# Kernel optimization log

Hardware: AMD Instinct MI355X
Metric: run time of the kernel (lower is better)

Reference implementation:

```python
import jax, jax.numpy as jnp
import numpy as np

NQ = 10          # qubits per register
DIM = 2 ** NQ    # 1024 amplitudes
N_CLS = 10       # canonical images (one per class)
N = 16384        # batch of samples
IMG = 28 * 28    # 784 pixels, zero-padded to DIM


def setup_inputs() -> dict:
    key = jax.random.key(0)
    k1, k2, k3 = jax.random.split(key, 3)
    z_re = jax.random.normal(k1, (N, DIM), dtype=jnp.float32)
    z_im = jax.random.normal(k2, (N, DIM), dtype=jnp.float32)
    # inputs are quantum states -> L2-normalize the complex vectors
    nrm = jnp.sqrt(jnp.sum(z_re * z_re + z_im * z_im, axis=1, keepdims=True))
    z_re = z_re / nrm
    z_im = z_im / nrm
    canon = jax.random.uniform(k3, (N_CLS, 1, 28, 28), dtype=jnp.float32)
    return {"z_re": z_re, "z_im": z_im, "canon": canon}


def reference(z_re, z_im, canon):
    # reshape_norm_padding: flatten, zero-pad to 2^nq, L2-normalize (real amplitudes)
    ref = canon.reshape(N_CLS, IMG)
    ref = jnp.pad(ref, ((0, 0), (0, DIM - IMG)))                  # [C, DIM]
    ref = ref / jnp.linalg.norm(ref, axis=1, keepdims=True)
    # Swap test: <Z_anc> = |<val|ref>|^2. ref is real, so with val = z_re + i*z_im:
    #   <val|ref> = (z_re @ ref^T) - i*(z_im @ ref^T)
    s_re = jnp.einsum('nd,cd->nc', z_re, ref)                     # [N, C]
    s_im = jnp.einsum('nd,cd->nc', z_im, ref)                     # [N, C]
    return s_re * s_re + s_im * s_im                              # [N, C] float32
```

## Files before the change

### kernel.cpp

```cpp
#include <hip/hip_runtime.h>

#define DIM     1024
#define N_CLS   10
#define NROWS   16384
#define IMG     784

#define NF4      196
#define NF4_PAD  224
#define NSTEP    7
#define LSTRIDE  224

#define WAVES_PER_BLK 8
#define ROWS_PER_BLK  16

typedef float f32x4 __attribute__((ext_vector_type(4)));
typedef float f32x2 __attribute__((ext_vector_type(2)));

static __device__ __forceinline__ f32x2 lo2(f32x4 v) {
  return __builtin_shufflevector(v, v, 0, 1);
}
static __device__ __forceinline__ f32x2 hi2(f32x4 v) {
  return __builtin_shufflevector(v, v, 2, 3);
}

static __device__ __forceinline__ void pk_fma(f32x2& acc, f32x2 a, f32x2 b) {
  asm("v_pk_fma_f32 %0, %1, %2, %0" : "+v"(acc) : "v"(a), "v"(b));
}

#define DPP_ADD(ctrl, rmask, bmask)                                           \
  x += __int_as_float(__builtin_amdgcn_update_dpp(                            \
      0, __float_as_int(x), ctrl, rmask, bmask, true));

__device__ __forceinline__ float wave64_sum(float x) {
  DPP_ADD(0x111, 0xf, 0xf)
  DPP_ADD(0x112, 0xf, 0xf)
  DPP_ADD(0x114, 0xf, 0xe)
  DPP_ADD(0x118, 0xf, 0xc)
  DPP_ADD(0x142, 0xa, 0xf)
  DPP_ADD(0x143, 0xc, 0xf)
  return x;
}

__device__ __forceinline__ float group32_sum(float x) {
  DPP_ADD(0x111, 0xf, 0xf)
  DPP_ADD(0x112, 0xf, 0xf)
  DPP_ADD(0x114, 0xf, 0xe)
  DPP_ADD(0x118, 0xf, 0xc)
  DPP_ADD(0x142, 0xa, 0xf)
  return x;
}
#undef DPP_ADD

__global__ __launch_bounds__(512, 8) void swaptest_kernel(
    const float* __restrict__ zre, const float* __restrict__ zim,
    const float* __restrict__ canon, float* __restrict__ out) {
  __shared__ f32x4 lref[N_CLS * LSTRIDE];

  const int t = threadIdx.x;
  const int lane = t & 63;
  const int wave = t >> 6;

#pragma unroll
  for (int c = 0; c < N_CLS; ++c) {
    if (t < NF4_PAD) {
      f32x4 v = {0.f, 0.f, 0.f, 0.f};
      if (t < NF4) v = ((const f32x4*)canon)[c * NF4 + t];
      lref[c * LSTRIDE + t] = v;
    }
  }
  __syncthreads();

  for (int c = wave; c < N_CLS; c += WAVES_PER_BLK) {
    float ss = 0.f;
    for (int i = lane; i < NF4_PAD; i += 64) {
      f32x4 v = lref[c * LSTRIDE + i];
      ss += v.x * v.x + v.y * v.y + v.z * v.z + v.w * v.w;
    }
    ss = wave64_sum(ss);
    float inv = __shfl(1.0f / sqrtf(ss), 63);
    for (int i = lane; i < NF4_PAD; i += 64) {
      f32x4 v = lref[c * LSTRIDE + i];
      v.x *= inv; v.y *= inv; v.z *= inv; v.w *= inv;
      lref[c * LSTRIDE + i] = v;
    }
  }
  __syncthreads();

  const int s = lane & 31;
  const int g = lane >> 5;
  const int row = blockIdx.x * ROWS_PER_BLK + wave * 2 + g;

  const f32x4* pr = (const f32x4*)(zre + ((size_t)row << 10)) + s;
  const f32x4* pi = (const f32x4*)(zim + ((size_t)row << 10)) + s;

  f32x2 accr[N_CLS], acci[N_CLS];
#pragma unroll
  for (int c = 0; c < N_CLS; ++c) {
    accr[c] = (f32x2){0.f, 0.f};
    acci[c] = (f32x2){0.f, 0.f};
  }

#pragma unroll
  for (int j = 0; j < NSTEP; ++j) {
    f32x4 zr = {0.f, 0.f, 0.f, 0.f};
    f32x4 zi = {0.f, 0.f, 0.f, 0.f};
    if (j < NSTEP - 1 || s < 16) {
      zr = pr[j * 32];
      zi = pi[j * 32];
    }
#pragma unroll
    for (int c = 0; c < N_CLS; ++c) {
      const f32x4 rv = lref[c * LSTRIDE + j * 32 + s];
      pk_fma(accr[c], lo2(zr), lo2(rv));
      pk_fma(accr[c], hi2(zr), hi2(rv));
      pk_fma(acci[c], lo2(zi), lo2(rv));
      pk_fma(acci[c], hi2(zi), hi2(rv));
    }
  }

#pragma unroll
  for (int c = 0; c < N_CLS; ++c) {
    float sr = group32_sum(accr[c].x + accr[c].y);
    float si = group32_sum(acci[c].x + acci[c].y);
    if (s == 31) {
      out[(size_t)row * N_CLS + c] = sr * sr + si * si;
    }
  }
}

extern "C" void kernel_launch(void* const* d_in, const int* in_sizes, int n_in,
                              void* d_out, int out_size, void* d_ws,
                              size_t ws_size, hipStream_t stream) {
  const float* z_re = (const float*)d_in[0];
  const float* z_im = (const float*)d_in[1];
  const float* canon = (const float*)d_in[2];
  float* out = (float*)d_out;
  (void)d_ws; (void)ws_size;

  const int nblk = NROWS / ROWS_PER_BLK;
  swaptest_kernel<<<nblk, 512, 0, stream>>>(z_re, z_im, canon, out);
}
```

Measured before the change: 153.8 us.

## Keep normalized reference vectors in registers and stream multiple rows per wave

Each wave now handles 8 rows with a full 64-lane split over the 784-element row (4 chunks of float4). It loads all reference chunks into registers once, so the per-row LDS reads go away. Loads for the next row are issued before the current row's FMAs to prefetch it. Blocks shrink to 4 waves with launch bounds of 256 threads and 2 blocks minimum. The kernel now holds 160 VGPRs of reference data plus prefetch buffers, so fewer waves fit per SIMD and there are fewer blocks in the grid. Each row reduction becomes a full 64-lane DPP sum.

New measurement: 152.0 us. Within noise of the previous version (-1.2%).

```diff
diff --git a/kernel.cpp b/kernel.cpp
--- a/kernel.cpp
+++ b/kernel.cpp
@@ -5,13 +5,12 @@
 #define NROWS   16384
 #define IMG     784
 
-#define NF4      196
-#define NF4_PAD  224
-#define NSTEP    7
-#define LSTRIDE  224
+#define NF4       196
+#define NCHUNK    4
+#define LSTRIDE   256
 
-#define WAVES_PER_BLK 8
-#define ROWS_PER_BLK  16
+#define WAVES_PER_BLK 4
+#define ROWS_PER_WAVE 8
 
 typedef float f32x4 __attribute__((ext_vector_type(4)));
 typedef float f32x2 __attribute__((ext_vector_type(2)));
@@ -27,31 +26,21 @@
   asm("v_pk_fma_f32 %0, %1, %2, %0" : "+v"(acc) : "v"(a), "v"(b));
 }
 
+__device__ __forceinline__ float wave64_sum(float x) {
 #define DPP_ADD(ctrl, rmask, bmask)                                           \
   x += __int_as_float(__builtin_amdgcn_update_dpp(                            \
       0, __float_as_int(x), ctrl, rmask, bmask, true));
-
-__device__ __forceinline__ float wave64_sum(float x) {
   DPP_ADD(0x111, 0xf, 0xf)
   DPP_ADD(0x112, 0xf, 0xf)
   DPP_ADD(0x114, 0xf, 0xe)
   DPP_ADD(0x118, 0xf, 0xc)
   DPP_ADD(0x142, 0xa, 0xf)
   DPP_ADD(0x143, 0xc, 0xf)
+#undef DPP_ADD
   return x;
 }
 
-__device__ __forceinline__ float group32_sum(float x) {
-  DPP_ADD(0x111, 0xf, 0xf)
-  DPP_ADD(0x112, 0xf, 0xf)
-  DPP_ADD(0x114, 0xf, 0xe)
-  DPP_ADD(0x118, 0xf, 0xc)
-  DPP_ADD(0x142, 0xa, 0xf)
-  return x;
-}
-#undef DPP_ADD
-
-__global__ __launch_bounds__(512, 8) void swaptest_kernel(
+__global__ __launch_bounds__(256, 2) void swaptest_kernel(
     const float* __restrict__ zre, const float* __restrict__ zim,
     const float* __restrict__ canon, float* __restrict__ out) {
   __shared__ f32x4 lref[N_CLS * LSTRIDE];
@@ -62,68 +51,90 @@
 
 #pragma unroll
   for (int c = 0; c < N_CLS; ++c) {
-    if (t < NF4_PAD) {
-      f32x4 v = {0.f, 0.f, 0.f, 0.f};
-      if (t < NF4) v = ((const f32x4*)canon)[c * NF4 + t];
-      lref[c * LSTRIDE + t] = v;
-    }
+    f32x4 v = {0.f, 0.f, 0.f, 0.f};
+    if (t < NF4) v = ((const f32x4*)canon)[c * NF4 + t];
+    lref[c * LSTRIDE + t] = v;
   }
   __syncthreads();
 
   for (int c = wave; c < N_CLS; c += WAVES_PER_BLK) {
     float ss = 0.f;
-    for (int i = lane; i < NF4_PAD; i += 64) {
-      f32x4 v = lref[c * LSTRIDE + i];
+#pragma unroll
+    for (int j = 0; j < LSTRIDE / 64; ++j) {
+      f32x4 v = lref[c * LSTRIDE + j * 64 + lane];
       ss += v.x * v.x + v.y * v.y + v.z * v.z + v.w * v.w;
     }
     ss = wave64_sum(ss);
     float inv = __shfl(1.0f / sqrtf(ss), 63);
-    for (int i = lane; i < NF4_PAD; i += 64) {
-      f32x4 v = lref[c * LSTRIDE + i];
+#pragma unroll
+    for (int j = 0; j < LSTRIDE / 64; ++j) {
+      f32x4 v = lref[c * LSTRIDE + j * 64 + lane];
       v.x *= inv; v.y *= inv; v.z *= inv; v.w *= inv;
-      lref[c * LSTRIDE + i] = v;
+      lref[c * LSTRIDE + j * 64 + lane] = v;
     }
   }
   __syncthreads();
 
-  const int s = lane & 31;
-  const int g = lane >> 5;
-  const int row = blockIdx.x * ROWS_PER_BLK + wave * 2 + g;
-
-  const f32x4* pr = (const f32x4*)(zre + ((size_t)row << 10)) + s;
-  const f32x4* pi = (const f32x4*)(zim + ((size_t)row << 10)) + s;
-
-  f32x2 accr[N_CLS], acci[N_CLS];
+  f32x4 refv[NCHUNK][N_CLS];
 #pragma unroll
-  for (int c = 0; c < N_CLS; ++c) {
-    accr[c] = (f32x2){0.f, 0.f};
-    acci[c] = (f32x2){0.f, 0.f};
+  for (int k = 0; k < NCHUNK; ++k) {
+#pragma unroll
+    for (int c = 0; c < N_CLS; ++c) {
+      refv[k][c] = lref[c * LSTRIDE + k * 64 + lane];
+    }
   }
 
+  const int wrow0 = (blockIdx.x * WAVES_PER_BLK + wave) * ROWS_PER_WAVE;
+  const f32x4* pr = (const f32x4*)zre + ((size_t)wrow0 << 8) + lane;
+  const f32x4* pi = (const f32x4*)zim + ((size_t)wrow0 << 8) + lane;
+  const bool tail = (lane < 16);
+
+  f32x4 bzr[NCHUNK], bzi[NCHUNK];
 #pragma unroll
-  for (int j = 0; j < NSTEP; ++j) {
-    f32x4 zr = {0.f, 0.f, 0.f, 0.f};
-    f32x4 zi = {0.f, 0.f, 0.f, 0.f};
-    if (j < NSTEP - 1 || s < 16) {
-      zr = pr[j * 32];
-      zi = pi[j * 32];
-    }
-#pragma unroll
-    for (int c = 0; c < N_CLS; ++c) {
-      const f32x4 rv = lref[c * LSTRIDE + j * 32 + s];
-      pk_fma(accr[c], lo2(zr), lo2(rv));
-      pk_fma(accr[c], hi2(zr), hi2(rv));
-      pk_fma(acci[c], lo2(zi), lo2(rv));
-      pk_fma(acci[c], hi2(zi), hi2(rv));
+  for (int k = 0; k < NCHUNK; ++k) {
+    bzr[k] = (f32x4){0.f, 0.f, 0.f, 0.f};
+    bzi[k] = (f32x4){0.f, 0.f, 0.f, 0.f};
+    if (k < NCHUNK - 1 || tail) {
+      bzr[k] = pr[k * 64];
+      bzi[k] = pi[k * 64];
     }
   }
 
 #pragma unroll
-  for (int c = 0; c < N_CLS; ++c) {
-    float sr = group32_sum(accr[c].x + accr[c].y);
-    float si = group32_sum(acci[c].x + acci[c].y);
-    if (s == 31) {
-      out[(size_t)row * N_CLS + c] = sr * sr + si * si;
+  for (int r = 0; r < ROWS_PER_WAVE; ++r) {
+    f32x2 accr[N_CLS], acci[N_CLS];
+#pragma unroll
+    for (int c = 0; c < N_CLS; ++c) {
+      accr[c] = (f32x2){0.f, 0.f};
+      acci[c] = (f32x2){0.f, 0.f};
+    }
+
+#pragma unroll
+    for (int k = 0; k < NCHUNK; ++k) {
+      const f32x4 zr = bzr[k];
+      const f32x4 zi = bzi[k];
+      if (r + 1 < ROWS_PER_WAVE && (k < NCHUNK - 1 || tail)) {
+        bzr[k] = pr[(size_t)(r + 1) * 256 + k * 64];
+        bzi[k] = pi[(size_t)(r + 1) * 256 + k * 64];
+      }
+#pragma unroll
+      for (int c = 0; c < N_CLS; ++c) {
+        const f32x4 rv = refv[k][c];
+        pk_fma(accr[c], lo2(zr), lo2(rv));
+        pk_fma(accr[c], hi2(zr), hi2(rv));
+        pk_fma(acci[c], lo2(zi), lo2(rv));
+        pk_fma(acci[c], hi2(zi), hi2(rv));
+      }
+    }
+
+    const int row = wrow0 + r;
+#pragma unroll
+    for (int c = 0; c < N_CLS; ++c) {
+      float sr = wave64_sum(accr[c].x + accr[c].y);
+      float si = wave64_sum(acci[c].x + acci[c].y);
+      if (lane == 63) {
+        out[(size_t)row * N_CLS + c] = sr * sr + si * si;
+      }
     }
   }
 }
@@ -137,6 +148,7 @@
   float* out = (float*)d_out;
   (void)d_ws; (void)ws_size;
 
-  const int nblk = NROWS / ROWS_PER_BLK;
-  swaptest_kernel<<<nblk, 512, 0, stream>>>(z_re, z_im, canon, out);
+  const int nblk = NROWS / (WAVES_PER_BLK * ROWS_PER_WAVE);
+  swaptest_kernel<<<nblk, 64 * WAVES_PER_BLK, 0, stream>>>(z_re, z_im, canon,
+                                                           out);
 }
```

## Double-buffer row pairs into LDS with async global loads per wave

Applied to the files above, without the earlier changes.

Each block now has four waves, and each wave loops over eight row pairs instead of handling a single pair. The next two pairs of real and imaginary rows are staged into a per-wave double buffer in LDS with global_load_lds, and `s_waitcnt vmcnt` keeps about one pair of loads in flight while the current pair is computed. The goal is more outstanding memory traffic per CU, hiding load latency in what is a bandwidth-bound streaming kernel. In exchange, LDS use rises to about 150KB, which allows one block per CU. The extra redundant stage on the final iteration and the counter-based waits that also count output stores may make some waits more conservative than needed.

Result: no change. 154.9 us (+0.7%).

```diff
diff --git a/kernel.cpp b/kernel.cpp
--- a/kernel.cpp
+++ b/kernel.cpp
@@ -1,17 +1,17 @@
 #include <hip/hip_runtime.h>
 
-#define DIM     1024
-#define N_CLS   10
-#define NROWS   16384
-#define IMG     784
+#define DIM    1024
+#define N_CLS  10
+#define NROWS  16384
+#define IMG    784
 
-#define NF4      196
-#define NF4_PAD  224
-#define NSTEP    7
-#define LSTRIDE  224
-
-#define WAVES_PER_BLK 8
-#define ROWS_PER_BLK  16
+#define NF4    196
+#define NLOAD  208
+#define NPAD   224
+#define NSTEP  7
+#define WAVES  4
+#define RP     8
+#define ROWS_PER_BLK (WAVES * 2 * RP)
 
 typedef float f32x4 __attribute__((ext_vector_type(4)));
 typedef float f32x2 __attribute__((ext_vector_type(2)));
@@ -26,6 +26,11 @@
 static __device__ __forceinline__ void pk_fma(f32x2& acc, f32x2 a, f32x2 b) {
   asm("v_pk_fma_f32 %0, %1, %2, %0" : "+v"(acc) : "v"(a), "v"(b));
 }
+
+#define ASYNC16(lds, g)                                                       \
+  __builtin_amdgcn_global_load_lds(                                           \
+      (const __attribute__((address_space(1))) unsigned int*)(g),             \
+      (__attribute__((address_space(3))) unsigned int*)(lds), 16, 0, 0)
 
 #define DPP_ADD(ctrl, rmask, bmask)                                           \
   x += __int_as_float(__builtin_amdgcn_update_dpp(                            \
@@ -51,81 +56,118 @@
 }
 #undef DPP_ADD
 
-__global__ __launch_bounds__(512, 8) void swaptest_kernel(
+__global__ __launch_bounds__(256, 1) void swaptest_kernel(
     const float* __restrict__ zre, const float* __restrict__ zim,
     const float* __restrict__ canon, float* __restrict__ out) {
-  __shared__ f32x4 lref[N_CLS * LSTRIDE];
+  __shared__ f32x4 zbuf[WAVES][2][4][NPAD];
+  __shared__ f32x4 lref[N_CLS * NPAD];
 
   const int t = threadIdx.x;
   const int lane = t & 63;
   const int wave = t >> 6;
 
+  for (int i = t; i < WAVES * 2 * 4 * 16; i += 256) {
+    const int w = i >> 7, rem = i & 127;
+    const int sl = rem >> 6, cr = (rem >> 4) & 3, e = rem & 15;
+    zbuf[w][sl][cr][NLOAD + e] = (f32x4){0.f, 0.f, 0.f, 0.f};
+  }
+
 #pragma unroll
   for (int c = 0; c < N_CLS; ++c) {
-    if (t < NF4_PAD) {
+    if (t < NPAD) {
       f32x4 v = {0.f, 0.f, 0.f, 0.f};
       if (t < NF4) v = ((const f32x4*)canon)[c * NF4 + t];
-      lref[c * LSTRIDE + t] = v;
+      lref[c * NPAD + t] = v;
     }
   }
   __syncthreads();
 
-  for (int c = wave; c < N_CLS; c += WAVES_PER_BLK) {
+  for (int c = wave; c < N_CLS; c += WAVES) {
     float ss = 0.f;
-    for (int i = lane; i < NF4_PAD; i += 64) {
-      f32x4 v = lref[c * LSTRIDE + i];
+    for (int i = lane; i < NPAD; i += 64) {
+      f32x4 v = lref[c * NPAD + i];
       ss += v.x * v.x + v.y * v.y + v.z * v.z + v.w * v.w;
     }
     ss = wave64_sum(ss);
     float inv = __shfl(1.0f / sqrtf(ss), 63);
-    for (int i = lane; i < NF4_PAD; i += 64) {
-      f32x4 v = lref[c * LSTRIDE + i];
+    for (int i = lane; i < NPAD; i += 64) {
+      f32x4 v = lref[c * NPAD + i];
       v.x *= inv; v.y *= inv; v.z *= inv; v.w *= inv;
-      lref[c * LSTRIDE + i] = v;
+      lref[c * NPAD + i] = v;
     }
   }
   __syncthreads();
 
   const int s = lane & 31;
   const int g = lane >> 5;
-  const int row = blockIdx.x * ROWS_PER_BLK + wave * 2 + g;
+  const int brow = blockIdx.x * ROWS_PER_BLK;
 
-  const f32x4* pr = (const f32x4*)(zre + ((size_t)row << 10)) + s;
-  const f32x4* pi = (const f32x4*)(zim + ((size_t)row << 10)) + s;
+  auto stage_row = [&](f32x4* dst, const float* src) {
+    const char* gp = (const char*)src;
+#pragma unroll
+    for (int i = 0; i < 3; ++i)
+      ASYNC16(&dst[i * 64], gp + (size_t)(i * 64 + lane) * 16);
+    if (lane < 16) ASYNC16(&dst[192], gp + (size_t)(192 + lane) * 16);
+  };
+  auto stage_pair = [&](int slot, int q) {
+    const int r0 = brow + q * (WAVES * 2) + wave * 2;
+    stage_row(&zbuf[wave][slot][0][0], zre + (size_t)r0 * DIM);
+    stage_row(&zbuf[wave][slot][1][0], zim + (size_t)r0 * DIM);
+    stage_row(&zbuf[wave][slot][2][0], zre + (size_t)(r0 + 1) * DIM);
+    stage_row(&zbuf[wave][slot][3][0], zim + (size_t)(r0 + 1) * DIM);
+  };
 
-  f32x2 accr[N_CLS], acci[N_CLS];
+  stage_pair(0, 0);
+  stage_pair(1, 1);
+
+  for (int r = 0; r < RP; ++r) {
+    asm volatile("s_waitcnt vmcnt(16)" ::: "memory");
+    __builtin_amdgcn_sched_barrier(0);
+
+    const int slot = r & 1;
+    const f32x4* zr_p = &zbuf[wave][slot][g * 2 + 0][0];
+    const f32x4* zi_p = &zbuf[wave][slot][g * 2 + 1][0];
+
+    f32x2 accr[N_CLS], acci[N_CLS];
 #pragma unroll
-  for (int c = 0; c < N_CLS; ++c) {
-    accr[c] = (f32x2){0.f, 0.f};
-    acci[c] = (f32x2){0.f, 0.f};
+    for (int c = 0; c < N_CLS; ++c) {
+      accr[c] = (f32x2){0.f, 0.f};
+      acci[c] = (f32x2){0.f, 0.f};
+    }
+
+#pragma unroll
+    for (int j = 0; j < NSTEP; ++j) {
+      const f32x4 zr = zr_p[j * 32 + s];
+      const f32x4 zi = zi_p[j * 32 + s];
+#pragma unroll
+      for (int c = 0; c < N_CLS; ++c) {
+        const f32x4 rv = lref[c * NPAD + j * 32 + s];
+        pk_fma(accr[c], lo2(zr), lo2(rv));
+        pk_fma(accr[c], hi2(zr), hi2(rv));
+        pk_fma(acci[c], lo2(zi), lo2(rv));
+        pk_fma(acci[c], hi2(zi), hi2(rv));
+      }
+    }
+
+    const int row0 = brow + r * (WAVES * 2) + wave * 2;
+#pragma unroll
+    for (int c = 0; c < N_CLS; ++c) {
+      float sr = group32_sum(accr[c].x + accr[c].y);
+      float si = group32_sum(acci[c].x + acci[c].y);
+      if (s == 31) {
+        out[(size_t)(row0 + g) * N_CLS + c] = sr * sr + si * si;
+      }
+    }
+
+    __builtin_amdgcn_sched_barrier(0);
+    if (r <= RP - 2) {
+      const int q = (r <= RP - 3) ? (r + 2) : (RP - 2);
+      stage_pair(slot, q);
+    }
+    __builtin_amdgcn_sched_barrier(0);
   }
 
-#pragma unroll
-  for (int j = 0; j < NSTEP; ++j) {
-    f32x4 zr = {0.f, 0.f, 0.f, 0.f};
-    f32x4 zi = {0.f, 0.f, 0.f, 0.f};
-    if (j < NSTEP - 1 || s < 16) {
-      zr = pr[j * 32];
-      zi = pi[j * 32];
-    }
-#pragma unroll
-    for (int c = 0; c < N_CLS; ++c) {
-      const f32x4 rv = lref[c * LSTRIDE + j * 32 + s];
-      pk_fma(accr[c], lo2(zr), lo2(rv));
-      pk_fma(accr[c], hi2(zr), hi2(rv));
-      pk_fma(acci[c], lo2(zi), lo2(rv));
-      pk_fma(acci[c], hi2(zi), hi2(rv));
-    }
-  }
-
-#pragma unroll
-  for (int c = 0; c < N_CLS; ++c) {
-    float sr = group32_sum(accr[c].x + accr[c].y);
-    float si = group32_sum(acci[c].x + acci[c].y);
-    if (s == 31) {
-      out[(size_t)row * N_CLS + c] = sr * sr + si * si;
-    }
-  }
+  asm volatile("s_waitcnt vmcnt(0)" ::: "memory");
 }
 
 extern "C" void kernel_launch(void* const* d_in, const int* in_sizes, int n_in,
@@ -138,5 +180,5 @@
   (void)d_ws; (void)ws_size;
 
   const int nblk = NROWS / ROWS_PER_BLK;
-  swaptest_kernel<<<nblk, 512, 0, stream>>>(z_re, z_im, canon, out);
+  swaptest_kernel<<<nblk, 64 * WAVES, 0, stream>>>(z_re, z_im, canon, out);
 }
```
